# Optimization experiments

Measured on AMD Instinct MI355X. Metric: run time of the kernel, lower is better.

## Reference

```python
import jax, jax.numpy as jnp
import numpy as np

N, IN_DIM, HID, LAT, E = 8192, 512, 256, 128, 262144


def gcn_conv(x, W, b, src, dst, n):
    # PyG-style GCNConv: linear transform, add self-loops, D^-1/2 A D^-1/2 aggregation, bias.
    h = x @ W                                                  # [n, out]
    loops = jnp.arange(n)
    s = jnp.concatenate([src, loops])
    d = jnp.concatenate([dst, loops])
    deg = jax.ops.segment_sum(jnp.ones(s.shape[0], x.dtype), d, num_segments=n)
    dinv = jnp.where(deg > 0, jax.lax.rsqrt(deg), jnp.zeros((), x.dtype))
    norm = dinv[s] * dinv[d]                                   # [E+n]
    out = jax.ops.segment_sum(h[s] * norm[:, None], d, num_segments=n)
    return out + b


def setup_inputs() -> dict:
    key = jax.random.key(0)
    ks = jax.random.split(key, 9)
    x = jax.random.normal(ks[0], (N, IN_DIM), dtype=jnp.float32)
    edge_index = jax.random.randint(ks[1], (2, E), 0, N, dtype=jnp.int64)
    eps = jax.random.normal(ks[2], (N, LAT), dtype=jnp.float32)
    # Glorot-ish scaled params
    W1 = jax.random.normal(ks[3], (IN_DIM, HID), dtype=jnp.float32) / np.sqrt(IN_DIM)
    b1 = jnp.zeros((HID,), jnp.float32)
    Wmu = jax.random.normal(ks[4], (HID, LAT), dtype=jnp.float32) / np.sqrt(HID)
    bmu = jnp.zeros((LAT,), jnp.float32)
    Wls = jax.random.normal(ks[5], (HID, LAT), dtype=jnp.float32) / np.sqrt(HID)
    bls = jnp.zeros((LAT,), jnp.float32)
    return {"x": x, "edge_index": edge_index, "eps": eps,
            "W1": W1, "b1": b1, "Wmu": Wmu, "bmu": bmu, "Wls": Wls, "bls": bls}


def reference(x, edge_index, eps, W1, b1, Wmu, bmu, Wls, bls):
    src, dst = edge_index[0], edge_index[1]
    n = x.shape[0]
    h = jax.nn.relu(gcn_conv(x, W1, b1, src, dst, n))          # [N, HID]
    mu = gcn_conv(h, Wmu, bmu, src, dst, n)                    # [N, LAT]
    logstd = gcn_conv(h, Wls, bls, src, dst, n)                # [N, LAT]
    z = eps * jnp.exp(logstd) + mu                             # reparametrize (training mode)
    adj_recon = jax.nn.sigmoid(z @ z.T)                        # [N, N]
    return adj_recon, mu, logstd
```

## Files before the change

kernel.cpp:

```cpp
#include <hip/hip_runtime.h>

#define N_NODES 8192
#define IN_DIM  512
#define HID     256
#define LAT     128
#define NEDGE   262144

typedef __attribute__((ext_vector_type(8)))  short  bf16x8;
typedef __attribute__((ext_vector_type(4)))  float  f32x4;
typedef __attribute__((ext_vector_type(16))) float  f32x16;
typedef unsigned short u16;
typedef __attribute__((ext_vector_type(4))) unsigned short u16x4;

static __device__ inline u16 f2bf(float f) {
    unsigned u = __float_as_uint(f);
    unsigned r = (u + 0x7fffu + ((u >> 16) & 1u)) >> 16;
    return (u16)r;
}
static __device__ inline float bf2f(u16 s) {
    return __uint_as_float(((unsigned)s) << 16);
}

#define PREP_BLOCKS 5888

static __device__ inline void convw_body(const float* __restrict__ W,
                                         u16* __restrict__ th,
                                         u16* __restrict__ tl,
                                         int K, int N, int Kld, int roff, int e) {
    if (e >= K * N) return;
    int k = e / N, n = e - k * N;
    float f = W[e];
    u16 hi = f2bf(f);
    u16 lo = f2bf(f - bf2f(hi));
    size_t o = (size_t)(roff + n) * Kld + k;
    th[o] = hi;
    tl[o] = lo;
}

__global__ __launch_bounds__(256) void prep_kernel(const int* __restrict__ dst,
                                                   int* __restrict__ cnt,
                                                   const float* __restrict__ X,
                                                   u16* __restrict__ xh,
                                                   u16* __restrict__ xl,
                                                   const float* __restrict__ W1,
                                                   u16* __restrict__ w1h,
                                                   u16* __restrict__ w1l,
                                                   const float* __restrict__ Wmu,
                                                   const float* __restrict__ Wls,
                                                   u16* __restrict__ wch,
                                                   u16* __restrict__ wcl) {
    const int b = blockIdx.x, t = threadIdx.x;
    if (b < 1024) {
        int e = b * 256 + t;
        atomicAdd(&cnt[dst[e]], 1);
    } else if (b < 5120) {
        int idx = (b - 1024) * 256 + t;
        f32x4 v = *(const f32x4*)(X + (size_t)idx * 4);
        u16x4 h, l;
#pragma unroll
        for (int j = 0; j < 4; ++j) {
            h[j] = f2bf(v[j]);
            l[j] = f2bf(v[j] - bf2f(h[j]));
        }
        *(u16x4*)(xh + (size_t)idx * 4) = h;
        *(u16x4*)(xl + (size_t)idx * 4) = l;
    } else if (b < 5632) {
        convw_body(W1, w1h, w1l, IN_DIM, HID, IN_DIM, 0, (b - 5120) * 256 + t);
    } else if (b < 5760) {
        convw_body(Wmu, wch, wcl, HID, LAT, HID, 0, (b - 5632) * 256 + t);
    } else {
        convw_body(Wls, wch, wcl, HID, LAT, HID, LAT, (b - 5760) * 256 + t);
    }
}

__global__ __launch_bounds__(256) void scan_kernel(const int* __restrict__ cnt,
                                                   int* __restrict__ rowptr,
                                                   int* __restrict__ cursor,
                                                   float* __restrict__ dinv) {
    __shared__ int part[256];
    const int t = threadIdx.x;
    const int base = t * 32;
    int local[32];
    int s = 0;
#pragma unroll
    for (int i = 0; i < 32; ++i) {
        int cv = cnt[base + i];
        local[i] = s; s += cv;
        dinv[base + i] = rsqrtf((float)cv + 1.0f);
    }
    part[t] = s;
    __syncthreads();
    for (int off = 1; off < 256; off <<= 1) {
        int v = 0;
        if (t >= off) v = part[t - off];
        __syncthreads();
        if (t >= off) part[t] += v;
        __syncthreads();
    }
    int pre = (t == 0) ? 0 : part[t - 1];
#pragma unroll
    for (int i = 0; i < 32; ++i) {
        int r = pre + local[i];
        rowptr[base + i] = r;
        cursor[base + i] = r;
    }
    if (t == 255) rowptr[8192] = part[255];
}

static __device__ inline void gemm_body(const u16* __restrict__ Ah,
                                        const u16* __restrict__ Al,
                                        const u16* __restrict__ Bth,
                                        const u16* __restrict__ Btl,
                                        float* __restrict__ C,
                                        int K, int ldc, int bx, int by, int tid) {
    const int lane = tid & 63;
    const int wave = tid >> 6;
    const int l16 = lane & 15, quad = lane >> 4;
    const int rowBase = by * 128 + (wave >> 1) * 64;
    const int colBase = bx * 128 + (wave & 1) * 64;

    f32x4 acc[4][4] = {};

    for (int k0 = 0; k0 < K; k0 += 32) {
        const int kk = k0 + quad * 8;
        bf16x8 ah[4], al[4], bh[4], bl[4];
#pragma unroll
        for (int r = 0; r < 4; ++r) {
            int row = rowBase + r * 16 + l16;
            ah[r] = *(const bf16x8*)(Ah + (size_t)row * K + kk);
            al[r] = *(const bf16x8*)(Al + (size_t)row * K + kk);
        }
#pragma unroll
        for (int c = 0; c < 4; ++c) {
            int row = colBase + c * 16 + l16;
            bh[c] = *(const bf16x8*)(Bth + (size_t)row * K + kk);
            bl[c] = *(const bf16x8*)(Btl + (size_t)row * K + kk);
        }
#pragma unroll
        for (int r = 0; r < 4; ++r)
#pragma unroll
            for (int c = 0; c < 4; ++c) {
                acc[r][c] = __builtin_amdgcn_mfma_f32_16x16x32_bf16(ah[r], bh[c], acc[r][c], 0, 0, 0);
                acc[r][c] = __builtin_amdgcn_mfma_f32_16x16x32_bf16(ah[r], bl[c], acc[r][c], 0, 0, 0);
                acc[r][c] = __builtin_amdgcn_mfma_f32_16x16x32_bf16(al[r], bh[c], acc[r][c], 0, 0, 0);
            }
    }

#pragma unroll
    for (int r = 0; r < 4; ++r)
#pragma unroll
        for (int c = 0; c < 4; ++c)
#pragma unroll
            for (int i = 0; i < 4; ++i) {
                int orow = rowBase + r * 16 + quad * 4 + i;
                int ocol = colBase + c * 16 + l16;
                C[(size_t)orow * ldc + ocol] = acc[r][c][i];
            }
}

__global__ __launch_bounds__(256) void fillgemm_kernel(const u16* __restrict__ xh,
                                                       const u16* __restrict__ xl,
                                                       const u16* __restrict__ w1h,
                                                       const u16* __restrict__ w1l,
                                                       float* __restrict__ pre1,
                                                       const int* __restrict__ src,
                                                       const int* __restrict__ dst,
                                                       int* __restrict__ cursor,
                                                       int* __restrict__ ebuf) {
    const int b = blockIdx.x;
    if (b < 128) {
        gemm_body(xh, xl, w1h, w1l, pre1, IN_DIM, HID, b & 1, b >> 1, threadIdx.x);
    } else {
        int e = (b - 128) * 256 + threadIdx.x;
        int pos = atomicAdd(&cursor[dst[e]], 1);
        ebuf[pos] = src[e];
    }
}

__global__ __launch_bounds__(256) void gemm2_kernel(const u16* __restrict__ h1h,
                                                    const u16* __restrict__ h1l,
                                                    const u16* __restrict__ wch,
                                                    const u16* __restrict__ wcl,
                                                    float* __restrict__ pre2) {
    gemm_body(h1h, h1l, wch, wcl, pre2, HID, HID, blockIdx.x & 1, blockIdx.x >> 1, threadIdx.x);
}

__global__ __launch_bounds__(256) void gather1_kernel(const float* __restrict__ pre1,
                                                      u16* __restrict__ h1h,
                                                      u16* __restrict__ h1l,
                                                      const int* __restrict__ rowptr,
                                                      const int* __restrict__ ebuf,
                                                      const float* __restrict__ dinv,
                                                      const float* __restrict__ b1) {
    const int wave = threadIdx.x >> 6, lane = threadIdx.x & 63;
    const int v = blockIdx.x * 4 + wave;
    const int c = lane * 4;
    const float dv = dinv[v];
    f32x4 acc = *(const f32x4*)(pre1 + (size_t)v * HID + c);
    acc *= dv * dv;
    int i = rowptr[v], end = rowptr[v + 1];
    for (; i + 3 < end; i += 4) {
        int s0 = ebuf[i], s1 = ebuf[i + 1], s2 = ebuf[i + 2], s3 = ebuf[i + 3];
        float n0 = dv * dinv[s0], n1 = dv * dinv[s1];
        float n2 = dv * dinv[s2], n3 = dv * dinv[s3];
        f32x4 h0 = *(const f32x4*)(pre1 + (size_t)s0 * HID + c);
        f32x4 h1v = *(const f32x4*)(pre1 + (size_t)s1 * HID + c);
        f32x4 h2 = *(const f32x4*)(pre1 + (size_t)s2 * HID + c);
        f32x4 h3 = *(const f32x4*)(pre1 + (size_t)s3 * HID + c);
#pragma unroll
        for (int j = 0; j < 4; ++j)
            acc[j] += (n0 * h0[j] + n1 * h1v[j]) + (n2 * h2[j] + n3 * h3[j]);
    }
    for (; i + 1 < end; i += 2) {
        int s0 = ebuf[i], s1 = ebuf[i + 1];
        float n0 = dv * dinv[s0], n1 = dv * dinv[s1];
        f32x4 h0 = *(const f32x4*)(pre1 + (size_t)s0 * HID + c);
        f32x4 h1v = *(const f32x4*)(pre1 + (size_t)s1 * HID + c);
#pragma unroll
        for (int j = 0; j < 4; ++j) acc[j] += n0 * h0[j] + n1 * h1v[j];
    }
    if (i < end) {
        int s0 = ebuf[i];
        float n0 = dv * dinv[s0];
        f32x4 h0 = *(const f32x4*)(pre1 + (size_t)s0 * HID + c);
#pragma unroll
        for (int j = 0; j < 4; ++j) acc[j] += n0 * h0[j];
    }
    f32x4 bb = *(const f32x4*)(b1 + c);
    u16x4 hv, lv;
#pragma unroll
    for (int j = 0; j < 4; ++j) {
        float h = fmaxf(acc[j] + bb[j], 0.0f);
        hv[j] = f2bf(h);
        lv[j] = f2bf(h - bf2f(hv[j]));
    }
    *(u16x4*)(h1h + (size_t)v * HID + c) = hv;
    *(u16x4*)(h1l + (size_t)v * HID + c) = lv;
}

__global__ __launch_bounds__(256) void gather2_kernel(const float* __restrict__ pre2,
                                                      const int* __restrict__ rowptr,
                                                      const int* __restrict__ ebuf,
                                                      const float* __restrict__ dinv,
                                                      const float* __restrict__ bmu,
                                                      const float* __restrict__ bls,
                                                      const float* __restrict__ eps,
                                                      float* __restrict__ out_mu,
                                                      float* __restrict__ out_ls,
                                                      u16* __restrict__ zhi,
                                                      u16* __restrict__ zlo) {
    const int wave = threadIdx.x >> 6, lane = threadIdx.x & 63;
    const int v = blockIdx.x * 4 + wave;
    const int c = lane * 4;
    const float dv = dinv[v];
    f32x4 acc = *(const f32x4*)(pre2 + (size_t)v * HID + c);
    acc *= dv * dv;
    int i = rowptr[v], end = rowptr[v + 1];
    for (; i + 3 < end; i += 4) {
        int s0 = ebuf[i], s1 = ebuf[i + 1], s2 = ebuf[i + 2], s3 = ebuf[i + 3];
        float n0 = dv * dinv[s0], n1 = dv * dinv[s1];
        float n2 = dv * dinv[s2], n3 = dv * dinv[s3];
        f32x4 h0 = *(const f32x4*)(pre2 + (size_t)s0 * HID + c);
        f32x4 h1v = *(const f32x4*)(pre2 + (size_t)s1 * HID + c);
        f32x4 h2 = *(const f32x4*)(pre2 + (size_t)s2 * HID + c);
        f32x4 h3 = *(const f32x4*)(pre2 + (size_t)s3 * HID + c);
#pragma unroll
        for (int j = 0; j < 4; ++j)
            acc[j] += (n0 * h0[j] + n1 * h1v[j]) + (n2 * h2[j] + n3 * h3[j]);
    }
    for (; i + 1 < end; i += 2) {
        int s0 = ebuf[i], s1 = ebuf[i + 1];
        float n0 = dv * dinv[s0], n1 = dv * dinv[s1];
        f32x4 h0 = *(const f32x4*)(pre2 + (size_t)s0 * HID + c);
        f32x4 h1v = *(const f32x4*)(pre2 + (size_t)s1 * HID + c);
#pragma unroll
        for (int j = 0; j < 4; ++j) acc[j] += n0 * h0[j] + n1 * h1v[j];
    }
    if (i < end) {
        int s0 = ebuf[i];
        float n0 = dv * dinv[s0];
        f32x4 h0 = *(const f32x4*)(pre2 + (size_t)s0 * HID + c);
#pragma unroll
        for (int j = 0; j < 4; ++j) acc[j] += n0 * h0[j];
    }
    const float* bias = (lane < 32) ? (bmu + c) : (bls + (c - 128));
    f32x4 bb = *(const f32x4*)bias;
#pragma unroll
    for (int j = 0; j < 4; ++j) acc[j] += bb[j];

    f32x4 other;
#pragma unroll
    for (int j = 0; j < 4; ++j) other[j] = __shfl(acc[j], (lane + 32) & 63, 64);

    if (lane < 32) {
        int idx = v * LAT + c;
        f32x4 ep = *(const f32x4*)(eps + idx);
        __builtin_nontemporal_store(acc, (f32x4*)(out_mu + idx));
        u16x4 hv, lv;
#pragma unroll
        for (int j = 0; j < 4; ++j) {
            float z = ep[j] * __expf(other[j]) + acc[j];
            u16 hi = f2bf(z);
            hv[j] = hi;
            lv[j] = f2bf(z - bf2f(hi));
        }
        *(u16x4*)(zhi + idx) = hv;
        *(u16x4*)(zlo + idx) = lv;
    } else {
        int idx = v * LAT + (c - 128);
        __builtin_nontemporal_store(acc, (f32x4*)(out_ls + idx));
    }
}

#define NTRI 2080
__global__ __launch_bounds__(256) void zzt_kernel(const u16* __restrict__ zhi,
                                                  const u16* __restrict__ zlo,
                                                  float* __restrict__ out) {
    __shared__ float lds[4][32][68];
    const int lane = threadIdx.x & 63;
    const int wave = threadIdx.x >> 6;
    const int l16 = lane & 15, quad = lane >> 4;
    const int l32 = lane & 31, half = lane >> 5;

    int bid = (blockIdx.x & 7) * 260 + (blockIdx.x >> 3);
    int by = (int)((sqrtf(8.0f * (float)bid + 1.0f) - 1.0f) * 0.5f);
    while ((by + 1) * (by + 2) / 2 <= bid) ++by;
    while (by * (by + 1) / 2 > bid) --by;
    const int bx = bid - by * (by + 1) / 2;

    const int rowBase = by * 128 + (wave >> 1) * 64;
    const int colBase = bx * 128 + (wave & 1) * 64;

    f32x16 acc[2][2] = {};

#pragma unroll
    for (int k = 0; k < 8; ++k) {
        const int kk = k * 16 + half * 8;
        bf16x8 xh[2], xl[2], yh[2], yl[2];
#pragma unroll
        for (int r = 0; r < 2; ++r) {
            int row = rowBase + r * 32 + l32;
            xh[r] = *(const bf16x8*)(zhi + (size_t)row * LAT + kk);
            xl[r] = *(const bf16x8*)(zlo + (size_t)row * LAT + kk);
        }
#pragma unroll
        for (int cc = 0; cc < 2; ++cc) {
            int row = colBase + cc * 32 + l32;
            yh[cc] = *(const bf16x8*)(zhi + (size_t)row * LAT + kk);
            yl[cc] = *(const bf16x8*)(zlo + (size_t)row * LAT + kk);
        }
#pragma unroll
        for (int r = 0; r < 2; ++r)
#pragma unroll
            for (int cc = 0; cc < 2; ++cc) {
                acc[r][cc] = __builtin_amdgcn_mfma_f32_32x32x16_bf16(yh[cc], xh[r], acc[r][cc], 0, 0, 0);
                acc[r][cc] = __builtin_amdgcn_mfma_f32_32x32x16_bf16(yh[cc], xl[r], acc[r][cc], 0, 0, 0);
                acc[r][cc] = __builtin_amdgcn_mfma_f32_32x32x16_bf16(yl[cc], xh[r], acc[r][cc], 0, 0, 0);
            }
    }

#pragma unroll
    for (int r = 0; r < 2; ++r)
#pragma unroll
        for (int cc = 0; cc < 2; ++cc)
#pragma unroll
            for (int i = 0; i < 16; ++i)
                acc[r][cc][i] = 1.0f / (1.0f + __expf(-acc[r][cc][i]));

#pragma unroll
    for (int r = 0; r < 2; ++r) {
#pragma unroll
        for (int cc = 0; cc < 2; ++cc)
#pragma unroll
            for (int q = 0; q < 4; ++q) {
                f32x4 v = { acc[r][cc][q * 4 + 0], acc[r][cc][q * 4 + 1],
                            acc[r][cc][q * 4 + 2], acc[r][cc][q * 4 + 3] };
                *(f32x4*)&lds[wave][l32][cc * 32 + q * 8 + half * 4] = v;
            }
#pragma unroll
        for (int it = 0; it < 8; ++it) {
            f32x4 v = *(const f32x4*)&lds[wave][it * 4 + quad][l16 * 4];
            int orow = rowBase + r * 32 + it * 4 + quad;
            __builtin_nontemporal_store(v, (f32x4*)(out + (size_t)orow * N_NODES + colBase + l16 * 4));
        }
    }

    if (by != bx) {
#pragma unroll
        for (int cc = 0; cc < 2; ++cc) {
#pragma unroll
            for (int r = 0; r < 2; ++r)
#pragma unroll
                for (int q = 0; q < 4; ++q)
#pragma unroll
                    for (int t = 0; t < 4; ++t)
                        lds[wave][q * 8 + half * 4 + t][r * 32 + l32] = acc[r][cc][q * 4 + t];
#pragma unroll
            for (int it = 0; it < 8; ++it) {
                f32x4 v = *(const f32x4*)&lds[wave][it * 4 + quad][l16 * 4];
                int orow = colBase + cc * 32 + it * 4 + quad;
                __builtin_nontemporal_store(v, (f32x4*)(out + (size_t)orow * N_NODES + rowBase + l16 * 4));
            }
        }
    }
}

extern "C" void kernel_launch(void* const* d_in, const int* in_sizes, int n_in,
                              void* d_out, int out_size, void* d_ws, size_t ws_size,
                              hipStream_t stream) {
    const float* x   = (const float*)d_in[0];
    const int*   ei  = (const int*)d_in[1];
    const float* eps = (const float*)d_in[2];
    const float* W1  = (const float*)d_in[3];
    const float* b1  = (const float*)d_in[4];
    const float* Wmu = (const float*)d_in[5];
    const float* bmu = (const float*)d_in[6];
    const float* Wls = (const float*)d_in[7];
    const float* bls = (const float*)d_in[8];
    const int* src = ei;
    const int* dst = ei + NEDGE;

    float* out = (float*)d_out;
    float* pre1 = out;
    float* pre2 = out + 2097152;
    int*   ibase  = (int*)(out + 4194304);
    int*   cnt    = ibase;
    int*   rowptr = ibase + 8192;
    int*   cursor = ibase + 16385;
    int*   ebuf   = ibase + 24577;
    u16* xhi    = (u16*)(out + 4587520);
    u16* xlo    = (u16*)(out + 6684672);
    u16* h1hi   = (u16*)(out + 8781824);
    u16* h1lo   = (u16*)(out + 9830400);
    u16* w1thi  = (u16*)(out + 10878976);
    u16* w1tlo  = (u16*)(out + 11010048);
    u16* wcathi = (u16*)(out + 11141120);
    u16* wcatlo = (u16*)(out + 11173888);
    float* out_mu = out + 67108864;
    float* out_ls = out + 68157440;

    float* dinv = (float*)d_ws;
    u16* zhi = (u16*)((char*)d_ws + 32768);
    u16* zlo = (u16*)((char*)d_ws + 32768 + 2097152);

    hipMemsetAsync(cnt, 0, 8192 * sizeof(int), stream);

    prep_kernel<<<PREP_BLOCKS, 256, 0, stream>>>(dst, cnt, x, xhi, xlo,
                                                 W1, w1thi, w1tlo, Wmu, Wls, wcathi, wcatlo);

    scan_kernel<<<1, 256, 0, stream>>>(cnt, rowptr, cursor, dinv);

    fillgemm_kernel<<<128 + 1024, 256, 0, stream>>>(xhi, xlo, w1thi, w1tlo, pre1,
                                                    src, dst, cursor, ebuf);

    gather1_kernel<<<N_NODES / 4, 256, 0, stream>>>(pre1, h1hi, h1lo, rowptr, ebuf, dinv, b1);

    gemm2_kernel<<<128, 256, 0, stream>>>(h1hi, h1lo, wcathi, wcatlo, pre2);

    gather2_kernel<<<N_NODES / 4, 256, 0, stream>>>(pre2, rowptr, ebuf, dinv, bmu, bls, eps,
                                                    out_mu, out_ls, zhi, zlo);

    zzt_kernel<<<NTRI, 256, 0, stream>>>(zhi, zlo, out);
}
```

Baseline: 475.4 us.

## Vectorize prep/fill edge loads, unroll gathers by 8, use plain output stores

Prep and CSR-fill now handle four edges per thread with vector int loads, and weight conversion reads four floats at a time, which cuts the block count. The gather loops unroll to 8 edges so more independent loads are in flight. The adjacency output stores in zzt switch from nontemporal to ordinary stores. The hot part is the 256 MB adjacency write, and dropping the nontemporal hint changes cache behaviour there, which could help or hurt.

```diff
diff --git a/kernel.cpp b/kernel.cpp
--- a/kernel.cpp
+++ b/kernel.cpp
@@ -9,6 +9,7 @@
 typedef __attribute__((ext_vector_type(8)))  short  bf16x8;
 typedef __attribute__((ext_vector_type(4)))  float  f32x4;
 typedef __attribute__((ext_vector_type(16))) float  f32x16;
+typedef __attribute__((ext_vector_type(4)))  int    i32x4;
 typedef unsigned short u16;
 typedef __attribute__((ext_vector_type(4))) unsigned short u16x4;
 
@@ -21,20 +22,23 @@
     return __uint_as_float(((unsigned)s) << 16);
 }
 
-#define PREP_BLOCKS 5888
-
-static __device__ inline void convw_body(const float* __restrict__ W,
-                                         u16* __restrict__ th,
-                                         u16* __restrict__ tl,
-                                         int K, int N, int Kld, int roff, int e) {
-    if (e >= K * N) return;
-    int k = e / N, n = e - k * N;
-    float f = W[e];
-    u16 hi = f2bf(f);
-    u16 lo = f2bf(f - bf2f(hi));
-    size_t o = (size_t)(roff + n) * Kld + k;
-    th[o] = hi;
-    tl[o] = lo;
+#define PREP_BLOCKS 4544
+
+static __device__ inline void convw4_body(const float* __restrict__ W,
+                                          u16* __restrict__ th,
+                                          u16* __restrict__ tl,
+                                          int N, int Kld, int roff, int e4) {
+    const int npack = N >> 2;
+    int k = e4 / npack, nb = (e4 - k * npack) * 4;
+    f32x4 v = *(const f32x4*)(W + (size_t)k * N + nb);
+#pragma unroll
+    for (int j = 0; j < 4; ++j) {
+        u16 hi = f2bf(v[j]);
+        u16 lo = f2bf(v[j] - bf2f(hi));
+        size_t o = (size_t)(roff + nb + j) * Kld + k;
+        th[o] = hi;
+        tl[o] = lo;
+    }
 }
 
 __global__ __launch_bounds__(256) void prep_kernel(const int* __restrict__ dst,
@@ -50,11 +54,13 @@
                                                    u16* __restrict__ wch,
                                                    u16* __restrict__ wcl) {
     const int b = blockIdx.x, t = threadIdx.x;
-    if (b < 1024) {
-        int e = b * 256 + t;
-        atomicAdd(&cnt[dst[e]], 1);
-    } else if (b < 5120) {
-        int idx = (b - 1024) * 256 + t;
+    if (b < 256) {
+        int e = (b * 256 + t) * 4;
+        i32x4 d4 = *(const i32x4*)(dst + e);
+#pragma unroll
+        for (int j = 0; j < 4; ++j) atomicAdd(&cnt[d4[j]], 1);
+    } else if (b < 4352) {
+        int idx = (b - 256) * 256 + t;
         f32x4 v = *(const f32x4*)(X + (size_t)idx * 4);
         u16x4 h, l;
 #pragma unroll
@@ -64,12 +70,12 @@
         }
         *(u16x4*)(xh + (size_t)idx * 4) = h;
         *(u16x4*)(xl + (size_t)idx * 4) = l;
-    } else if (b < 5632) {
-        convw_body(W1, w1h, w1l, IN_DIM, HID, IN_DIM, 0, (b - 5120) * 256 + t);
-    } else if (b < 5760) {
-        convw_body(Wmu, wch, wcl, HID, LAT, HID, 0, (b - 5632) * 256 + t);
+    } else if (b < 4480) {
+        convw4_body(W1, w1h, w1l, HID, IN_DIM, 0, (b - 4352) * 256 + t);
+    } else if (b < 4512) {
+        convw4_body(Wmu, wch, wcl, LAT, HID, 0, (b - 4480) * 256 + t);
     } else {
-        convw_body(Wls, wch, wcl, HID, LAT, HID, LAT, (b - 5760) * 256 + t);
+        convw4_body(Wls, wch, wcl, LAT, HID, LAT, (b - 4512) * 256 + t);
     }
 }
 
@@ -171,9 +177,14 @@
     if (b < 128) {
         gemm_body(xh, xl, w1h, w1l, pre1, IN_DIM, HID, b & 1, b >> 1, threadIdx.x);
     } else {
-        int e = (b - 128) * 256 + threadIdx.x;
-        int pos = atomicAdd(&cursor[dst[e]], 1);
-        ebuf[pos] = src[e];
+        int e = ((b - 128) * 256 + threadIdx.x) * 4;
+        i32x4 s4 = *(const i32x4*)(src + e);
+        i32x4 d4 = *(const i32x4*)(dst + e);
+#pragma unroll
+        for (int j = 0; j < 4; ++j) {
+            int pos = atomicAdd(&cursor[d4[j]], 1);
+            ebuf[pos] = s4[j];
+        }
     }
 }
 
@@ -199,17 +210,20 @@
     f32x4 acc = *(const f32x4*)(pre1 + (size_t)v * HID + c);
     acc *= dv * dv;
     int i = rowptr[v], end = rowptr[v + 1];
-    for (; i + 3 < end; i += 4) {
-        int s0 = ebuf[i], s1 = ebuf[i + 1], s2 = ebuf[i + 2], s3 = ebuf[i + 3];
-        float n0 = dv * dinv[s0], n1 = dv * dinv[s1];
-        float n2 = dv * dinv[s2], n3 = dv * dinv[s3];
-        f32x4 h0 = *(const f32x4*)(pre1 + (size_t)s0 * HID + c);
-        f32x4 h1v = *(const f32x4*)(pre1 + (size_t)s1 * HID + c);
-        f32x4 h2 = *(const f32x4*)(pre1 + (size_t)s2 * HID + c);
-        f32x4 h3 = *(const f32x4*)(pre1 + (size_t)s3 * HID + c);
-#pragma unroll
-        for (int j = 0; j < 4; ++j)
-            acc[j] += (n0 * h0[j] + n1 * h1v[j]) + (n2 * h2[j] + n3 * h3[j]);
+    for (; i + 7 < end; i += 8) {
+        int s[8];
+        float n[8];
+        f32x4 h[8];
+#pragma unroll
+        for (int j = 0; j < 8; ++j) s[j] = ebuf[i + j];
+#pragma unroll
+        for (int j = 0; j < 8; ++j) n[j] = dv * dinv[s[j]];
+#pragma unroll
+        for (int j = 0; j < 8; ++j) h[j] = *(const f32x4*)(pre1 + (size_t)s[j] * HID + c);
+#pragma unroll
+        for (int j = 0; j < 8; ++j)
+#pragma unroll
+            for (int q = 0; q < 4; ++q) acc[q] += n[j] * h[j][q];
     }
     for (; i + 1 < end; i += 2) {
         int s0 = ebuf[i], s1 = ebuf[i + 1];
@@ -256,17 +270,20 @@
     f32x4 acc = *(const f32x4*)(pre2 + (size_t)v * HID + c);
     acc *= dv * dv;
     int i = rowptr[v], end = rowptr[v + 1];
-    for (; i + 3 < end; i += 4) {
-        int s0 = ebuf[i], s1 = ebuf[i + 1], s2 = ebuf[i + 2], s3 = ebuf[i + 3];
-        float n0 = dv * dinv[s0], n1 = dv * dinv[s1];
-        float n2 = dv * dinv[s2], n3 = dv * dinv[s3];
-        f32x4 h0 = *(const f32x4*)(pre2 + (size_t)s0 * HID + c);
-        f32x4 h1v = *(const f32x4*)(pre2 + (size_t)s1 * HID + c);
-        f32x4 h2 = *(const f32x4*)(pre2 + (size_t)s2 * HID + c);
-        f32x4 h3 = *(const f32x4*)(pre2 + (size_t)s3 * HID + c);
-#pragma unroll
-        for (int j = 0; j < 4; ++j)
-            acc[j] += (n0 * h0[j] + n1 * h1v[j]) + (n2 * h2[j] + n3 * h3[j]);
+    for (; i + 7 < end; i += 8) {
+        int s[8];
+        float n[8];
+        f32x4 h[8];
+#pragma unroll
+        for (int j = 0; j < 8; ++j) s[j] = ebuf[i + j];
+#pragma unroll
+        for (int j = 0; j < 8; ++j) n[j] = dv * dinv[s[j]];
+#pragma unroll
+        for (int j = 0; j < 8; ++j) h[j] = *(const f32x4*)(pre2 + (size_t)s[j] * HID + c);
+#pragma unroll
+        for (int j = 0; j < 8; ++j)
+#pragma unroll
+            for (int q = 0; q < 4; ++q) acc[q] += n[j] * h[j][q];
     }
     for (; i + 1 < end; i += 2) {
         int s0 = ebuf[i], s1 = ebuf[i + 1];
@@ -381,7 +398,7 @@
         for (int it = 0; it < 8; ++it) {
             f32x4 v = *(const f32x4*)&lds[wave][it * 4 + quad][l16 * 4];
             int orow = rowBase + r * 32 + it * 4 + quad;
-            __builtin_nontemporal_store(v, (f32x4*)(out + (size_t)orow * N_NODES + colBase + l16 * 4));
+            *(f32x4*)(out + (size_t)orow * N_NODES + colBase + l16 * 4) = v;
         }
     }
 
@@ -399,7 +416,7 @@
             for (int it = 0; it < 8; ++it) {
                 f32x4 v = *(const f32x4*)&lds[wave][it * 4 + quad][l16 * 4];
                 int orow = colBase + cc * 32 + it * 4 + quad;
-                __builtin_nontemporal_store(v, (f32x4*)(out + (size_t)orow * N_NODES + rowBase + l16 * 4));
+                *(f32x4*)(out + (size_t)orow * N_NODES + rowBase + l16 * 4) = v;
             }
         }
     }
@@ -450,8 +467,8 @@
 
     scan_kernel<<<1, 256, 0, stream>>>(cnt, rowptr, cursor, dinv);
 
-    fillgemm_kernel<<<128 + 1024, 256, 0, stream>>>(xhi, xlo, w1thi, w1tlo, pre1,
-                                                    src, dst, cursor, ebuf);
+    fillgemm_kernel<<<128 + 256, 256, 0, stream>>>(xhi, xlo, w1thi, w1tlo, pre1,
+                                                   src, dst, cursor, ebuf);
 
     gather1_kernel<<<N_NODES / 4, 256, 0, stream>>>(pre1, h1hi, h1lo, rowptr, ebuf, dinv, b1);
 
```

Result: slower. 487.7 us (+2.6%).
